# Performance work log

Measured on AMD Instinct MI355X. Metric: run time of the kernel, lower is better.

## Reference

```python
import jax, jax.numpy as jnp
import numpy as np

B, N, D = 8, 1024, 768
H, HD = 12, 64


def setup_inputs() -> dict:
    key = jax.random.key(0)
    ks = jax.random.split(key, 9)
    return {
        "x": jax.random.normal(ks[0], (B, N, D), dtype=jnp.float32),
        "Wq": jax.random.normal(ks[1], (H, HD, HD), dtype=jnp.float32) * (HD ** -0.5),
        "Wk": jax.random.normal(ks[2], (H, HD, HD), dtype=jnp.float32) * (HD ** -0.5),
        "Wv": jax.random.normal(ks[3], (H, HD, HD), dtype=jnp.float32) * (HD ** -0.5),
        "bq": jax.random.normal(ks[4], (H, HD), dtype=jnp.float32) * 0.02,
        "bk": jax.random.normal(ks[5], (H, HD), dtype=jnp.float32) * 0.02,
        "bv": jax.random.normal(ks[6], (H, HD), dtype=jnp.float32) * 0.02,
        "Wo": jax.random.normal(ks[7], (D, D), dtype=jnp.float32) * (D ** -0.5),
        "bo": jnp.zeros((D,), dtype=jnp.float32),
    }


def reference(x, Wq, Wk, Wv, bq, bk, bv, Wo, bo):
    # x: [B, N, D]; split into H heads of size HD along the feature dim
    b, n, d = x.shape
    h, hd = Wq.shape[0], Wq.shape[1]
    xh = x.reshape(b, n, h, hd)
    # per-head linear projections (stacked nn.Linear(head_dim, head_dim))
    q = jnp.einsum('bnhd,hde->bhne', xh, Wq) + bq[None, :, None, :]
    k = jnp.einsum('bnhd,hde->bhne', xh, Wk) + bk[None, :, None, :]
    v = jnp.einsum('bnhd,hde->bhne', xh, Wv) + bv[None, :, None, :]
    # NOTE: faithful quirk - scale uses FULL dim, not head_dim
    scale = d ** -0.5
    scores = jnp.einsum('bhid,bhjd->bhij', q, k) * scale  # [B,H,N,N]
    attn = jax.nn.softmax(scores, axis=-1)
    out = jnp.einsum('bhij,bhjd->bhid', attn, v)  # [B,H,N,HD]
    out = out.transpose(0, 2, 1, 3).reshape(b, n, d)  # concat heads
    return out @ Wo.T + bo  # wO: nn.Linear(dim, dim)
```

## Files before the change

kernel.cpp:

```cpp
#include <hip/hip_runtime.h>


typedef __attribute__((ext_vector_type(8))) short short8;
typedef __attribute__((ext_vector_type(4))) float floatx4;

#define MFMA16(a, b, c) __builtin_amdgcn_mfma_f32_16x16x32_bf16((a), (b), (c), 0, 0, 0)

#if __has_builtin(__builtin_amdgcn_exp2f)
#define EXP2(x) __builtin_amdgcn_exp2f(x)
#else
#define EXP2(x) __expf(0.6931471805599453f * (x))
#endif
#if __has_builtin(__builtin_amdgcn_rcpf)
#define RCP(x) __builtin_amdgcn_rcpf(x)
#else
#define RCP(x) (1.0f / (x))
#endif

__device__ __forceinline__ unsigned short f2bf(float f) {
    union { float f; unsigned int i; } c;
    c.f = f;
    unsigned int i = c.i;
    return (unsigned short)((i + 0x7fffu + ((i >> 16) & 1u)) >> 16);
}
__device__ __forceinline__ unsigned short f2bf_trunc(float f) {
    union { float f; unsigned int i; } c;
    c.f = f;
    return (unsigned short)(c.i >> 16);
}

__global__ __launch_bounds__(256) void prep_weights(
    const float* __restrict__ Wq, const float* __restrict__ Wk,
    const float* __restrict__ Wv, const float* __restrict__ Wo,
    unsigned short* __restrict__ Wqt, unsigned short* __restrict__ Wkt,
    unsigned short* __restrict__ Wvt, unsigned short* __restrict__ Wob)
{
    int tid = blockIdx.x * 256 + threadIdx.x;
    if (tid < 49152) {
        int h = tid >> 12, r = tid & 4095;
        int e = r >> 6, k = r & 63;
        int src = h * 4096 + k * 64 + e, dst = h * 4096 + e * 64 + k;
        Wqt[dst] = f2bf(Wq[src]);
        Wkt[dst] = f2bf(Wk[src]);
        Wvt[dst] = f2bf(Wv[src]);
    }
    for (int i = tid; i < 589824; i += 147456) Wob[i] = f2bf(Wo[i]);
}

__global__ __launch_bounds__(256) void qkv_proj(
    const float* __restrict__ x,
    const unsigned short* __restrict__ Wqt, const unsigned short* __restrict__ Wkt,
    const unsigned short* __restrict__ Wvt,
    const float* __restrict__ bq, const float* __restrict__ bk,
    const float* __restrict__ bv,
    unsigned short* __restrict__ Q, unsigned short* __restrict__ K,
    unsigned short* __restrict__ Vt)
{
    __shared__ __align__(16) unsigned short xlds[64 * 72];
    __shared__ __align__(16) unsigned short vlds[64 * 72];

    const int bh = blockIdx.y;
    const int b = bh / 12, h = bh % 12;
    const int wave = threadIdx.x >> 6, lane = threadIdx.x & 63;
    const int lrow = lane & 15, quad = lane >> 4;
    const int row0 = blockIdx.x * 64;
    const float scale = 0.052058776672f;

    {
        const int tr = threadIdx.x >> 4;
        const int tc = (threadIdx.x & 15) * 4;
        #pragma unroll
        for (int rr = 0; rr < 4; ++rr) {
            const int r = tr + rr * 16;
            const float* src = x + ((size_t)(b * 1024 + row0 + r)) * 768
                               + h * 64 + tc;
            float4 f = *(const float4*)src;
            unsigned short pkd[4];
            pkd[0] = f2bf(f.x); pkd[1] = f2bf(f.y);
            pkd[2] = f2bf(f.z); pkd[3] = f2bf(f.w);
            *(uint2*)&xlds[r * 72 + tc] = *(uint2*)pkd;
        }
    }
    __syncthreads();

    short8 xb0 = *(const short8*)&xlds[(wave * 16 + lrow) * 72 + quad * 8];
    short8 xb1 = *(const short8*)&xlds[(wave * 16 + lrow) * 72 + 32 + quad * 8];

    const floatx4 zero = { 0.f, 0.f, 0.f, 0.f };

    const unsigned short* Wm[2] = { Wqt + h * 4096, Wkt + h * 4096 };
    const float* bm[2] = { bq + h * 64, bk + h * 64 };
    unsigned short* Om[2] = {
        Q + ((size_t)bh * 1024 + row0 + wave * 16 + lrow) * 64,
        K + ((size_t)bh * 1024 + row0 + wave * 16 + lrow) * 64 };
    #pragma unroll
    for (int m = 0; m < 2; ++m) {
        const unsigned short* W = Wm[m];
        #pragma unroll
        for (int t = 0; t < 4; ++t) {
            short8 wa0 = *(const short8*)(W + (t * 16 + lrow) * 64 + quad * 8);
            short8 wa1 = *(const short8*)(W + (t * 16 + lrow) * 64 + 32 + quad * 8);
            floatx4 acc = zero;
            acc = MFMA16(wa0, xb0, acc);
            acc = MFMA16(wa1, xb1, acc);
            float4 bias = *(const float4*)(bm[m] + t * 16 + quad * 4);
            const float bs[4] = { bias.x, bias.y, bias.z, bias.w };
            unsigned short pkd[4];
            #pragma unroll
            for (int r = 0; r < 4; ++r) {
                float v = acc[r] + bs[r];
                if (m == 0) v *= scale;
                pkd[r] = f2bf(v);
            }
            *(uint2*)(Om[m] + t * 16 + quad * 4) = *(uint2*)pkd;
        }
    }

    {
        const unsigned short* W = Wvt + h * 4096;
        const float* bvh = bv + h * 64;
        #pragma unroll
        for (int t = 0; t < 4; ++t) {
            short8 wa0 = *(const short8*)(W + (t * 16 + lrow) * 64 + quad * 8);
            short8 wa1 = *(const short8*)(W + (t * 16 + lrow) * 64 + 32 + quad * 8);
            floatx4 acc = zero;
            acc = MFMA16(wa0, xb0, acc);
            acc = MFMA16(wa1, xb1, acc);
            float4 bias = *(const float4*)(bvh + t * 16 + quad * 4);
            const float bs[4] = { bias.x, bias.y, bias.z, bias.w };
            #pragma unroll
            for (int r = 0; r < 4; ++r)
                vlds[(t * 16 + quad * 4 + r) * 72 + wave * 16 + lrow]
                    = f2bf(acc[r] + bs[r]);
        }
    }
    __syncthreads();
    {
        const int er = threadIdx.x >> 2;
        const int sc = threadIdx.x & 3;
        short8 v0 = *(const short8*)&vlds[er * 72 + sc * 16];
        short8 v1 = *(const short8*)&vlds[er * 72 + sc * 16 + 8];
        unsigned short* dst = Vt + (size_t)bh * 65536 + (size_t)er * 1024
                              + row0 + sc * 16;
        *(short8*)dst = v0;
        *(short8*)(dst + 8) = v1;
    }
}

__global__ __launch_bounds__(256) void attn_kernel(
    const unsigned short* __restrict__ Q, const unsigned short* __restrict__ K,
    const unsigned short* __restrict__ Vt, unsigned short* __restrict__ AO)
{
    __shared__ __align__(16) unsigned short Klds[64 * 72];
    __shared__ __align__(16) unsigned short Vlds[64 * 72];

    const int bh = (int)blockIdx.x + ((int)blockIdx.y >> 3) * 8;
    const int qb = blockIdx.y & 7;
    const int b = bh / 12, h = bh % 12;
    const int wave = threadIdx.x >> 6, lane = threadIdx.x & 63;
    const int lrow = lane & 15, quad = lane >> 4;
    const int qrow0 = qb * 128 + wave * 32;

    const unsigned short* Qb = Q + (size_t)bh * 65536;
    const unsigned short* Kb = K + (size_t)bh * 65536;
    const unsigned short* Vb = Vt + (size_t)bh * 65536;

    const int tch = threadIdx.x & 7, trow = threadIdx.x >> 3;
    const int slot0 = ((trow & 4) << 2) | ((trow >> 3) << 2) | (trow & 3);

    short8 aq[2][2];
    #pragma unroll
    for (int mm = 0; mm < 2; ++mm) {
        const unsigned short* qr = Qb + (size_t)(qrow0 + mm * 16 + lrow) * 64;
        aq[mm][0] = *(const short8*)(qr + quad * 8);
        aq[mm][1] = *(const short8*)(qr + 32 + quad * 8);
    }

    const floatx4 zero = { 0.f, 0.f, 0.f, 0.f };
    float part[2] = { 0.f, 0.f };
    floatx4 Oacc[2][4];
    #pragma unroll
    for (int mm = 0; mm < 2; ++mm)
        #pragma unroll
        for (int t = 0; t < 4; ++t) Oacc[mm][t] = zero;

    short8 kpre[2], vpre[2];
    kpre[0] = *(const short8*)(Kb + (size_t)trow * 64 + tch * 8);
    kpre[1] = *(const short8*)(Kb + (size_t)(trow + 32) * 64 + tch * 8);
    vpre[0] = *(const short8*)(Vb + (size_t)trow * 1024 + tch * 8);
    vpre[1] = *(const short8*)(Vb + (size_t)(trow + 32) * 1024 + tch * 8);

    for (int jt = 0; jt < 16; ++jt) {
        *(short8*)&Klds[slot0 * 72 + tch * 8] = kpre[0];
        *(short8*)&Klds[(slot0 + 32) * 72 + tch * 8] = kpre[1];
        *(short8*)&Vlds[trow * 72 + tch * 8] = vpre[0];
        *(short8*)&Vlds[(trow + 32) * 72 + tch * 8] = vpre[1];
        __syncthreads();

        {
            const int jn = ((jt + 1) & 15) * 64;
            kpre[0] = *(const short8*)(Kb + (size_t)(jn + trow) * 64 + tch * 8);
            kpre[1] = *(const short8*)(Kb + (size_t)(jn + trow + 32) * 64 + tch * 8);
            vpre[0] = *(const short8*)(Vb + (size_t)trow * 1024 + jn + tch * 8);
            vpre[1] = *(const short8*)(Vb + (size_t)(trow + 32) * 1024 + jn + tch * 8);
        }

        #pragma unroll
        for (int w = 0; w < 2; ++w) {
            short8 kA[2][2];
            #pragma unroll
            for (int tau = 0; tau < 2; ++tau) {
                int kr = w * 32 + tau * 16 + lrow;
                kA[tau][0] = *(const short8*)&Klds[kr * 72 + quad * 8];
                kA[tau][1] = *(const short8*)&Klds[kr * 72 + 32 + quad * 8];
            }
            short8 vA[4];
            #pragma unroll
            for (int t = 0; t < 4; ++t)
                vA[t] = *(const short8*)&Vlds[(t * 16 + lrow) * 72
                                              + w * 32 + quad * 8];

            #pragma unroll
            for (int mm = 0; mm < 2; ++mm) {
                floatx4 s0 = zero, s1 = zero;
                s0 = MFMA16(kA[0][0], aq[mm][0], s0);
                s0 = MFMA16(kA[0][1], aq[mm][1], s0);
                s1 = MFMA16(kA[1][0], aq[mm][0], s1);
                s1 = MFMA16(kA[1][1], aq[mm][1], s1);

                short8 pk;
                #pragma unroll
                for (int r = 0; r < 4; ++r) {
                    float p0 = EXP2(s0[r]);
                    float p1 = EXP2(s1[r]);
                    part[mm] += p0 + p1;
                    pk[r] = (short)f2bf_trunc(p0);
                    pk[4 + r] = (short)f2bf_trunc(p1);
                }
                #pragma unroll
                for (int t = 0; t < 4; ++t)
                    Oacc[mm][t] = MFMA16(vA[t], pk, Oacc[mm][t]);
            }
        }
        __syncthreads();
    }

    #pragma unroll
    for (int mm = 0; mm < 2; ++mm) {
        float ts = part[mm];
        ts += __shfl_xor(ts, 16);
        ts += __shfl_xor(ts, 32);
        float inv = RCP(ts);
        unsigned short* orow = AO
            + ((size_t)(b * 1024 + qrow0 + mm * 16 + lrow)) * 768 + h * 64;
        #pragma unroll
        for (int t = 0; t < 4; ++t) {
            unsigned short pkd[4];
            #pragma unroll
            for (int r = 0; r < 4; ++r)
                pkd[r] = f2bf(Oacc[mm][t][r] * inv);
            *(uint2*)(orow + t * 16 + quad * 4) = *(uint2*)pkd;
        }
    }
}

__global__ __launch_bounds__(256) void out_proj(
    const unsigned short* __restrict__ AO, const unsigned short* __restrict__ Wob,
    const float* __restrict__ bo, float* __restrict__ Y)
{
    __shared__ __align__(16) unsigned short Alds[2][128 * 72];
    __shared__ __align__(16) unsigned short Blds[2][96 * 72];

    const int wave = threadIdx.x >> 6, lane = threadIdx.x & 63;
    const int lrow = lane & 15, quad = lane >> 4;
    const int row0 = blockIdx.x * 128;
    const int c0 = blockIdx.y * 96;
    const int wrow = (wave >> 1) * 64, wcol = (wave & 1) * 48;

    const int tch = threadIdx.x & 7, trow = threadIdx.x >> 3;

    const floatx4 zero = { 0.f, 0.f, 0.f, 0.f };
    floatx4 acc[3][4];
    #pragma unroll
    for (int u = 0; u < 3; ++u)
        #pragma unroll
        for (int t = 0; t < 4; ++t) acc[u][t] = zero;

    short8 apre[4], bpre[3];
    #pragma unroll
    for (int rr = 0; rr < 4; ++rr)
        apre[rr] = *(const short8*)(AO + (size_t)(row0 + trow + rr * 32) * 768
                                    + tch * 8);
    #pragma unroll
    for (int rr = 0; rr < 3; ++rr)
        bpre[rr] = *(const short8*)(Wob + (size_t)(c0 + trow + rr * 32) * 768
                                    + tch * 8);
    #pragma unroll
    for (int rr = 0; rr < 4; ++rr)
        *(short8*)&Alds[0][(trow + rr * 32) * 72 + tch * 8] = apre[rr];
    #pragma unroll
    for (int rr = 0; rr < 3; ++rr)
        *(short8*)&Blds[0][(trow + rr * 32) * 72 + tch * 8] = bpre[rr];
    #pragma unroll
    for (int rr = 0; rr < 4; ++rr)
        apre[rr] = *(const short8*)(AO + (size_t)(row0 + trow + rr * 32) * 768
                                    + 64 + tch * 8);
    #pragma unroll
    for (int rr = 0; rr < 3; ++rr)
        bpre[rr] = *(const short8*)(Wob + (size_t)(c0 + trow + rr * 32) * 768
                                    + 64 + tch * 8);

    for (int jt = 0; jt < 12; ++jt) {
        __syncthreads();

        {
            const int nb = (jt + 1) & 1;
            #pragma unroll
            for (int rr = 0; rr < 4; ++rr)
                *(short8*)&Alds[nb][(trow + rr * 32) * 72 + tch * 8] = apre[rr];
            #pragma unroll
            for (int rr = 0; rr < 3; ++rr)
                *(short8*)&Blds[nb][(trow + rr * 32) * 72 + tch * 8] = bpre[rr];
        }
        {
            const int kn = (jt + 2 < 12) ? (jt + 2) * 64 : 0;
            #pragma unroll
            for (int rr = 0; rr < 4; ++rr)
                apre[rr] = *(const short8*)(AO
                    + (size_t)(row0 + trow + rr * 32) * 768 + kn + tch * 8);
            #pragma unroll
            for (int rr = 0; rr < 3; ++rr)
                bpre[rr] = *(const short8*)(Wob
                    + (size_t)(c0 + trow + rr * 32) * 768 + kn + tch * 8);
        }

        const unsigned short* ab = (const unsigned short*)Alds[jt & 1];
        const unsigned short* bb = (const unsigned short*)Blds[jt & 1];
        #pragma unroll
        for (int kc = 0; kc < 2; ++kc) {
            short8 aoF[4], wF[3];
            #pragma unroll
            for (int t = 0; t < 4; ++t)
                aoF[t] = *(const short8*)&ab[(wrow + t * 16 + lrow) * 72
                                             + kc * 32 + quad * 8];
            #pragma unroll
            for (int u = 0; u < 3; ++u)
                wF[u] = *(const short8*)&bb[(wcol + u * 16 + lrow) * 72
                                            + kc * 32 + quad * 8];
            #pragma unroll
            for (int u = 0; u < 3; ++u)
                #pragma unroll
                for (int t = 0; t < 4; ++t)
                    acc[u][t] = MFMA16(wF[u], aoF[t], acc[u][t]);
        }
    }

    #pragma unroll
    for (int u = 0; u < 3; ++u) {
        const int cb = c0 + wcol + u * 16 + quad * 4;
        float4 bias = *(const float4*)(bo + cb);
        const float bs[4] = { bias.x, bias.y, bias.z, bias.w };
        #pragma unroll
        for (int t = 0; t < 4; ++t) {
            const int row = row0 + wrow + t * 16 + lrow;
            float out[4];
            #pragma unroll
            for (int r = 0; r < 4; ++r) out[r] = acc[u][t][r] + bs[r];
            *(float4*)(Y + (size_t)row * 768 + cb) = *(float4*)out;
        }
    }
}

extern "C" void kernel_launch(void* const* d_in, const int* in_sizes, int n_in,
                              void* d_out, int out_size, void* d_ws, size_t ws_size,
                              hipStream_t stream)
{
    const float* x  = (const float*)d_in[0];
    const float* Wq = (const float*)d_in[1];
    const float* Wk = (const float*)d_in[2];
    const float* Wv = (const float*)d_in[3];
    const float* bq = (const float*)d_in[4];
    const float* bk = (const float*)d_in[5];
    const float* bv = (const float*)d_in[6];
    const float* Wo = (const float*)d_in[7];
    const float* bo = (const float*)d_in[8];

    unsigned short* Q   = (unsigned short*)d_ws;
    unsigned short* K   = Q + 6291456;
    unsigned short* Vt  = K + 6291456;
    unsigned short* AO  = Vt + 6291456;
    unsigned short* Wqt = AO + 6291456;
    unsigned short* Wkt = Wqt + 49152;
    unsigned short* Wvt = Wkt + 49152;
    unsigned short* Wob = Wvt + 49152;
    float* Y = (float*)d_out;

    prep_weights<<<dim3(576), 256, 0, stream>>>(Wq, Wk, Wv, Wo, Wqt, Wkt, Wvt, Wob);
    qkv_proj<<<dim3(16, 96), 256, 0, stream>>>(x, Wqt, Wkt, Wvt, bq, bk, bv, Q, K, Vt);
    attn_kernel<<<dim3(8, 96), 256, 0, stream>>>(Q, K, Vt, AO);
    out_proj<<<dim3(64, 8), 256, 0, stream>>>(AO, Wob, bo, Y);
}
```

Baseline: 166.0 us.

## Fuse weight preparation into QKV projection kernel and drop the prep launch

Removes the separate prep_weights kernel. Each QKV block now converts and transposes its head's fp32 Wq/Wk/Wv into padded shared memory, and the grid as a whole converts Wo to bf16 with a grid-stride loop. This saves one kernel launch and a global round trip for the small transposed weights. In exchange, every block repeats the per-head weight conversion with scattered LDS stores and adds an extra barrier.

New measurement: 157.6 us. 5.1% less time.

```diff
diff --git a/kernel.cpp b/kernel.cpp
--- a/kernel.cpp
+++ b/kernel.cpp
@@ -29,35 +29,20 @@
     return (unsigned short)(c.i >> 16);
 }
 
-__global__ __launch_bounds__(256) void prep_weights(
-    const float* __restrict__ Wq, const float* __restrict__ Wk,
-    const float* __restrict__ Wv, const float* __restrict__ Wo,
-    unsigned short* __restrict__ Wqt, unsigned short* __restrict__ Wkt,
-    unsigned short* __restrict__ Wvt, unsigned short* __restrict__ Wob)
-{
-    int tid = blockIdx.x * 256 + threadIdx.x;
-    if (tid < 49152) {
-        int h = tid >> 12, r = tid & 4095;
-        int e = r >> 6, k = r & 63;
-        int src = h * 4096 + k * 64 + e, dst = h * 4096 + e * 64 + k;
-        Wqt[dst] = f2bf(Wq[src]);
-        Wkt[dst] = f2bf(Wk[src]);
-        Wvt[dst] = f2bf(Wv[src]);
-    }
-    for (int i = tid; i < 589824; i += 147456) Wob[i] = f2bf(Wo[i]);
-}
-
 __global__ __launch_bounds__(256) void qkv_proj(
     const float* __restrict__ x,
-    const unsigned short* __restrict__ Wqt, const unsigned short* __restrict__ Wkt,
-    const unsigned short* __restrict__ Wvt,
+    const float* __restrict__ Wq, const float* __restrict__ Wk,
+    const float* __restrict__ Wv,
     const float* __restrict__ bq, const float* __restrict__ bk,
     const float* __restrict__ bv,
+    const float* __restrict__ Wo, unsigned short* __restrict__ Wob,
     unsigned short* __restrict__ Q, unsigned short* __restrict__ K,
     unsigned short* __restrict__ Vt)
 {
-    __shared__ __align__(16) unsigned short xlds[64 * 72];
-    __shared__ __align__(16) unsigned short vlds[64 * 72];
+    __shared__ __align__(16) unsigned short smem[4 * 4608];
+    unsigned short* const wlds = smem;
+    unsigned short* const xlds = smem;
+    unsigned short* const vlds = smem + 3 * 4608;
 
     const int bh = blockIdx.y;
     const int b = bh / 12, h = bh % 12;
@@ -65,6 +50,11 @@
     const int lrow = lane & 15, quad = lane >> 4;
     const int row0 = blockIdx.x * 64;
     const float scale = 0.052058776672f;
+
+    {
+        const int gtid = (blockIdx.y * 16 + blockIdx.x) * 256 + threadIdx.x;
+        for (int i = gtid; i < 589824; i += 393216) Wob[i] = f2bf(Wo[i]);
+    }
 
     {
         const int tr = threadIdx.x >> 4;
@@ -85,21 +75,40 @@
 
     short8 xb0 = *(const short8*)&xlds[(wave * 16 + lrow) * 72 + quad * 8];
     short8 xb1 = *(const short8*)&xlds[(wave * 16 + lrow) * 72 + 32 + quad * 8];
+    __syncthreads();
+
+    {
+        const float* Wsrc[3] = { Wq + h * 4096, Wk + h * 4096, Wv + h * 4096 };
+        #pragma unroll
+        for (int m = 0; m < 3; ++m) {
+            unsigned short* wd = wlds + m * 4608;
+            #pragma unroll
+            for (int i = 0; i < 4; ++i) {
+                const int f = i * 256 + threadIdx.x;
+                float4 v = *(const float4*)(Wsrc[m] + f * 4);
+                const int k = f >> 4, e0 = (f & 15) << 2;
+                wd[(e0 + 0) * 72 + k] = f2bf(v.x);
+                wd[(e0 + 1) * 72 + k] = f2bf(v.y);
+                wd[(e0 + 2) * 72 + k] = f2bf(v.z);
+                wd[(e0 + 3) * 72 + k] = f2bf(v.w);
+            }
+        }
+    }
+    __syncthreads();
 
     const floatx4 zero = { 0.f, 0.f, 0.f, 0.f };
 
-    const unsigned short* Wm[2] = { Wqt + h * 4096, Wkt + h * 4096 };
     const float* bm[2] = { bq + h * 64, bk + h * 64 };
     unsigned short* Om[2] = {
         Q + ((size_t)bh * 1024 + row0 + wave * 16 + lrow) * 64,
         K + ((size_t)bh * 1024 + row0 + wave * 16 + lrow) * 64 };
     #pragma unroll
     for (int m = 0; m < 2; ++m) {
-        const unsigned short* W = Wm[m];
+        const unsigned short* W = wlds + m * 4608;
         #pragma unroll
         for (int t = 0; t < 4; ++t) {
-            short8 wa0 = *(const short8*)(W + (t * 16 + lrow) * 64 + quad * 8);
-            short8 wa1 = *(const short8*)(W + (t * 16 + lrow) * 64 + 32 + quad * 8);
+            short8 wa0 = *(const short8*)(W + (t * 16 + lrow) * 72 + quad * 8);
+            short8 wa1 = *(const short8*)(W + (t * 16 + lrow) * 72 + 32 + quad * 8);
             floatx4 acc = zero;
             acc = MFMA16(wa0, xb0, acc);
             acc = MFMA16(wa1, xb1, acc);
@@ -117,12 +126,12 @@
     }
 
     {
-        const unsigned short* W = Wvt + h * 4096;
+        const unsigned short* W = wlds + 2 * 4608;
         const float* bvh = bv + h * 64;
         #pragma unroll
         for (int t = 0; t < 4; ++t) {
-            short8 wa0 = *(const short8*)(W + (t * 16 + lrow) * 64 + quad * 8);
-            short8 wa1 = *(const short8*)(W + (t * 16 + lrow) * 64 + 32 + quad * 8);
+            short8 wa0 = *(const short8*)(W + (t * 16 + lrow) * 72 + quad * 8);
+            short8 wa1 = *(const short8*)(W + (t * 16 + lrow) * 72 + 32 + quad * 8);
             floatx4 acc = zero;
             acc = MFMA16(wa0, xb0, acc);
             acc = MFMA16(wa1, xb1, acc);
@@ -389,14 +398,11 @@
     unsigned short* K   = Q + 6291456;
     unsigned short* Vt  = K + 6291456;
     unsigned short* AO  = Vt + 6291456;
-    unsigned short* Wqt = AO + 6291456;
-    unsigned short* Wkt = Wqt + 49152;
-    unsigned short* Wvt = Wkt + 49152;
-    unsigned short* Wob = Wvt + 49152;
+    unsigned short* Wob = AO + 6291456;
     float* Y = (float*)d_out;
 
-    prep_weights<<<dim3(576), 256, 0, stream>>>(Wq, Wk, Wv, Wo, Wqt, Wkt, Wvt, Wob);
-    qkv_proj<<<dim3(16, 96), 256, 0, stream>>>(x, Wqt, Wkt, Wvt, bq, bk, bv, Q, K, Vt);
+    qkv_proj<<<dim3(16, 96), 256, 0, stream>>>(x, Wq, Wk, Wv, bq, bk, bv,
+                                               Wo, Wob, Q, K, Vt);
     attn_kernel<<<dim3(8, 96), 256, 0, stream>>>(Q, K, Vt, AO);
     out_proj<<<dim3(64, 8), 256, 0, stream>>>(AO, Wob, bo, Y);
 }
```
